# Kernel optimization log

Measured on AMD Instinct MI355X. Metric: run time of the kernel, lower is better.

## Reference

```python
import jax, jax.numpy as jnp
import numpy as np

NEG = -1e30  # mask value safe for logsumexp/max
HALF_POS = 4   # positive window: [t-4, t+4)
HALF_ALL = 16  # combined window: [t-16, t+16) (pos + 12 negatives each side)


def _normalize(x, axis=-1, eps=1e-12):
    # matches torch F.normalize: x / max(||x||, eps)
    n = jnp.linalg.norm(x, axis=axis, keepdims=True)
    return x / jnp.maximum(n, eps)


def _banded_logits(q, k, temperature):
    # q, k: [B, T, D] (normalized). Returns logits [B, T, W], valid mask, pos mask.
    B, T, D = q.shape
    offsets = jnp.arange(-HALF_ALL, HALF_ALL)          # [W=32]
    j = jnp.arange(T)[:, None] + offsets[None, :]      # [T, W] absolute indices
    valid = (j >= 0) & (j < T)                         # combined (pos+neg) window
    jc = jnp.clip(j, 0, T - 1)
    kg = k[:, jc, :]                                   # [B, T, W, D]
    logits = jnp.einsum('btd,btwd->btw', q, kg) / temperature
    pos = valid & (offsets >= -HALF_POS)[None, :] & (offsets < HALF_POS)[None, :]
    return logits, valid, pos


def _direction(q, k, temperature):
    logits, valid, pos = _banded_logits(q, k, temperature)
    lse_all = jax.nn.logsumexp(jnp.where(valid, logits, NEG), axis=2)  # [B, T]
    lse_pos = jax.nn.logsumexp(jnp.where(pos, logits, NEG), axis=2)    # [B, T]
    # per-t loss is mean over batch; summed over t
    loss_sum = jnp.sum(jnp.mean(lse_all - lse_pos, axis=0))
    max_all = jnp.max(jnp.where(valid, logits, NEG), axis=2)
    max_pos = jnp.max(jnp.where(pos, logits, NEG), axis=2)
    # argmax falls in positive block (positives listed first -> ties go positive)
    correct = jnp.sum((max_pos >= max_all).astype(jnp.float32))
    return loss_sum, correct


def setup_inputs() -> dict:
    key = jax.random.key(0)
    k1, k2 = jax.random.split(key)
    B, T, D = 16, 4096, 128
    return {
        'motion_feature': jax.random.normal(k1, (B, T, D), dtype=jnp.float32),
        'audio_feature': jax.random.normal(k2, (B, T, D), dtype=jnp.float32),
    }


def reference(motion_feature, audio_feature):
    temperature = 0.1
    B, T, D = motion_feature.shape
    m = _normalize(motion_feature, axis=2)
    a = _normalize(audio_feature, axis=2)
    m2a_loss, m2a_correct = _direction(m, a, temperature)
    a2m_loss, a2m_correct = _direction(a, m, temperature)
    final_loss = (m2a_loss + a2m_loss) / (2 * T)
    total_correct = (m2a_correct + a2m_correct) / (2 * T * B)
    return final_loss, total_correct
```

## Files before the change

kernel.cpp:

```cpp
#include <hip/hip_runtime.h>
#include <hip/hip_bf16.h>

typedef __attribute__((ext_vector_type(8))) short bf16x8;
typedef __attribute__((ext_vector_type(4))) float f32x4;

#define T_DIM 4096
#define B_DIM 16
#define D_DIM 128
#define TILE 64
#define NTILE 4
#define ROWS 96
#define SROW 136
#define TBUF (ROWS * SROW)
#define NEGV -1e30f
#define NBLK 256
#define SCALE (1.0f / 131072.0f)

#define LDS_BARRIER() asm volatile("s_waitcnt lgkmcnt(0)\n\ts_barrier" ::: "memory")

__global__ __launch_bounds__(512, 2) void lcl_main(
    const float* __restrict__ mot, const float* __restrict__ aud,
    float* __restrict__ ws)
{
    __shared__ unsigned short sbuf[2 * 2 * TBUF];
    __shared__ float redL[8], redC[8];

    const int tid  = threadIdx.x;
    const int lane = tid & 63;
    const int wv   = tid >> 6;
    const int g32  = tid >> 5;
    const int l32  = tid & 31;

    const int lin = blockIdx.x;
    const int swz = (lin & 7) * (NBLK / 8) + (lin >> 3);
    const int by  = swz >> 4;
    const int tg  = swz & 15;
    const int tbase = tg * (NTILE * TILE);
    const size_t base = (size_t)by * (T_DIM * D_DIM);
    const bool edge = (tg == 0) || (tg == 15);

    const int dir = wv >> 2;
    const int mi  = wv & 3;

    const int fr    = lane & 15;
    const int fch   = (lane >> 4) * 8;
    const int col16 = lane & 15;
    const int g     = lane >> 4;

    float4 vm[6], va[6];
    auto issue = [&](int tstart) {
        const size_t off = base + (size_t)(tstart - 16 + g32) * D_DIM + l32 * 4;
        const float* spm = mot + off;
        const float* spa = aud + off;
        if (!edge) {
            #pragma unroll
            for (int i = 0; i < 6; ++i) {
                vm[i] = *reinterpret_cast<const float4*>(spm + (size_t)(16 * i) * D_DIM);
                va[i] = *reinterpret_cast<const float4*>(spa + (size_t)(16 * i) * D_DIM);
            }
        } else {
            #pragma unroll
            for (int i = 0; i < 6; ++i) {
                const bool ok = (unsigned)(tstart - 16 + g32 + 16 * i) < (unsigned)T_DIM;
                vm[i] = make_float4(0.f, 0.f, 0.f, 0.f);
                va[i] = vm[i];
                if (ok) {
                    vm[i] = *reinterpret_cast<const float4*>(spm + (size_t)(16 * i) * D_DIM);
                    va[i] = *reinterpret_cast<const float4*>(spa + (size_t)(16 * i) * D_DIM);
                }
            }
        }
    };

    issue(tbase);

    float lossW = 0.f, corrW = 0.f;

    #pragma unroll
    for (int tile = 0; tile < NTILE; ++tile) {
        const int t0  = tbase + tile * TILE;
        const int cur = tile & 1;
        unsigned short* smc = sbuf + (cur * 2 + 0) * TBUF;
        unsigned short* sac = sbuf + (cur * 2 + 1) * TBUF;

        {
            unsigned short* dpm = smc + g32 * SROW + l32 * 4;
            unsigned short* dpa = sac + g32 * SROW + l32 * 4;
            #pragma unroll
            for (int i = 0; i < 6; ++i) {
                union { __hip_bfloat16 h[4]; uint2 u; } pm, pa;
                pm.h[0] = __float2bfloat16(vm[i].x);
                pm.h[1] = __float2bfloat16(vm[i].y);
                pm.h[2] = __float2bfloat16(vm[i].z);
                pm.h[3] = __float2bfloat16(vm[i].w);
                pa.h[0] = __float2bfloat16(va[i].x);
                pa.h[1] = __float2bfloat16(va[i].y);
                pa.h[2] = __float2bfloat16(va[i].z);
                pa.h[3] = __float2bfloat16(va[i].w);
                *reinterpret_cast<uint2*>(dpm + 16 * i * SROW) = pm.u;
                *reinterpret_cast<uint2*>(dpa + 16 * i * SROW) = pa.u;
            }
        }

        if (tile + 1 < NTILE) issue(t0 + TILE);

        LDS_BARRIER();

        const unsigned short* q = (dir ? sac : smc);
        const unsigned short* k = (dir ? smc : sac);
        f32x4 acc0 = {0.f,0.f,0.f,0.f}, acc1 = acc0, acc2 = acc0;
        f32x4 n0 = acc0, n1 = acc0, n2 = acc0, nq = acc0;
        const unsigned short* qrow = q + (16 * (mi + 1) + fr) * SROW + fch;
        const unsigned short* k0   = k + ((mi + 0) * 16 + fr) * SROW + fch;
        const unsigned short* k1   = k + ((mi + 1) * 16 + fr) * SROW + fch;
        const unsigned short* k2   = k + ((mi + 2) * 16 + fr) * SROW + fch;
        #pragma unroll
        for (int ks = 0; ks < 4; ++ks) {
            bf16x8 bq = *reinterpret_cast<const bf16x8*>(qrow + ks * 32);
            bf16x8 a0 = *reinterpret_cast<const bf16x8*>(k0   + ks * 32);
            bf16x8 a1 = *reinterpret_cast<const bf16x8*>(k1   + ks * 32);
            bf16x8 a2 = *reinterpret_cast<const bf16x8*>(k2   + ks * 32);
            acc0 = __builtin_amdgcn_mfma_f32_16x16x32_bf16(a0, bq, acc0, 0, 0, 0);
            acc1 = __builtin_amdgcn_mfma_f32_16x16x32_bf16(a1, bq, acc1, 0, 0, 0);
            acc2 = __builtin_amdgcn_mfma_f32_16x16x32_bf16(a2, bq, acc2, 0, 0, 0);
            n0   = __builtin_amdgcn_mfma_f32_16x16x32_bf16(a0, a0, n0, 0, 0, 0);
            n1   = __builtin_amdgcn_mfma_f32_16x16x32_bf16(a1, a1, n1, 0, 0, 0);
            n2   = __builtin_amdgcn_mfma_f32_16x16x32_bf16(a2, a2, n2, 0, 0, 0);
            nq   = __builtin_amdgcn_mfma_f32_16x16x32_bf16(bq, bq, nq, 0, 0, 0);
        }

        const int rs = col16 & 3;
        const float dq = (rs == 0) ? nq[0] : (rs == 1) ? nq[1] : (rs == 2) ? nq[2] : nq[3];
        const float d0 = (rs == 0) ? n0[0] : (rs == 1) ? n0[1] : (rs == 2) ? n0[2] : n0[3];
        const float d1 = (rs == 0) ? n1[0] : (rs == 1) ? n1[1] : (rs == 2) ? n1[2] : n1[3];
        const float d2 = (rs == 0) ? n2[0] : (rs == 1) ? n2[1] : (rs == 2) ? n2[2] : n2[3];
        const float iq = rsqrtf(fmaxf(dq, 1e-24f));
        const float i0 = rsqrtf(fmaxf(d0, 1e-24f));
        const float i1 = rsqrtf(fmaxf(d1, 1e-24f));
        const float i2 = rsqrtf(fmaxf(d2, 1e-24f));

        const float scq10 = 10.0f * __shfl(iq, col16 + 16 * (col16 >> 2));
        const int srcn = 20 * g;
        f32x4 sck0, sck1, sck2;
        #pragma unroll
        for (int r = 0; r < 4; ++r) {
            sck0[r] = __shfl(i0, srcn + r);
            sck1[r] = __shfl(i1, srcn + r);
            sck2[r] = __shfl(i2, srcn + r);
        }

        const int jbase  = t0 - 16 + 16 * mi + 4 * g;
        const int kkbase = 4 * g - col16;

        float lv[12];
        bool  pmk[12];
        float mx = NEGV, mxp = NEGV;
        #pragma unroll
        for (int bb = 0; bb < 3; ++bb) {
            const f32x4 acc = (bb == 0) ? acc0 : ((bb == 1) ? acc1 : acc2);
            const f32x4 sck = (bb == 0) ? sck0 : ((bb == 1) ? sck1 : sck2);
            #pragma unroll
            for (int r = 0; r < 4; ++r) {
                const int kk = kkbase + 16 * bb + r;
                const int jg = jbase  + 16 * bb + r;
                const bool ok = ((unsigned)kk < 32u) && ((unsigned)jg < (unsigned)T_DIM);
                const float li = ok ? acc[r] * (scq10 * sck[r]) : NEGV;
                const bool  pi = ((unsigned)(kk - 12) < 8u);
                lv[bb * 4 + r]  = li;
                pmk[bb * 4 + r] = pi;
                mx  = fmaxf(mx, li);
                mxp = pi ? fmaxf(mxp, li) : mxp;
            }
        }
        mx  = fmaxf(mx,  __shfl_xor(mx,  16));
        mx  = fmaxf(mx,  __shfl_xor(mx,  32));
        mxp = fmaxf(mxp, __shfl_xor(mxp, 16));
        mxp = fmaxf(mxp, __shfl_xor(mxp, 32));

        float s = 0.f, sp = 0.f;
        #pragma unroll
        for (int i = 0; i < 12; ++i) {
            const float e = __expf(lv[i] - mx);
            s  += e;
            sp += pmk[i] ? e : 0.f;
        }
        s  += __shfl_xor(s,  16);  s  += __shfl_xor(s,  32);
        sp += __shfl_xor(sp, 16);  sp += __shfl_xor(sp, 32);

        if (g == 0) {
            lossW += __logf(s / sp);
            corrW += (mxp >= mx) ? 1.0f : 0.0f;
        }
    }

    #pragma unroll
    for (int m = 32; m; m >>= 1) {
        lossW += __shfl_xor(lossW, m);
        corrW += __shfl_xor(corrW, m);
    }
    if (lane == 0) { redL[wv] = lossW; redC[wv] = corrW; }
    __syncthreads();
    if (tid == 0) {
        float L = 0.f, C = 0.f;
        #pragma unroll
        for (int i = 0; i < 8; ++i) { L += redL[i]; C += redC[i]; }
        ws[2 * swz]     = L;
        ws[2 * swz + 1] = C;
    }
}

__global__ __launch_bounds__(256) void lcl_final(
    const float* __restrict__ ws, float* __restrict__ out)
{
    const int tid = threadIdx.x;
    const float2 v = reinterpret_cast<const float2*>(ws)[tid];
    float L = v.x, C = v.y;
    #pragma unroll
    for (int m = 32; m; m >>= 1) { L += __shfl_xor(L, m); C += __shfl_xor(C, m); }
    __shared__ float rl[4], rc[4];
    if ((tid & 63) == 0) { rl[tid >> 6] = L; rc[tid >> 6] = C; }
    __syncthreads();
    if (tid == 0) {
        out[0] = (rl[0] + rl[1] + rl[2] + rl[3]) * SCALE;
        out[1] = (rc[0] + rc[1] + rc[2] + rc[3]) * SCALE;
    }
}

extern "C" void kernel_launch(void* const* d_in, const int* in_sizes, int n_in,
                              void* d_out, int out_size, void* d_ws, size_t ws_size,
                              hipStream_t stream) {
    const float* mot = (const float*)d_in[0];
    const float* aud = (const float*)d_in[1];
    float* out = (float*)d_out;
    float* ws  = (float*)d_ws;

    lcl_main<<<NBLK, 512, 0, stream>>>(mot, aud, ws);
    lcl_final<<<1, 256, 0, stream>>>(ws, out);
}
```

Measured before the change: 21.44 us.

## Double block count with half tiles per block and single-buffered LDS

Splits the time axis into 32 groups per batch instead of 16, so 512 blocks each process 2 tiles rather than 256 blocks processing 4. The LDS double buffer is dropped for one buffer per input, with an extra barrier after the MFMA loads so the next tile's stores cannot overwrite data still being read. The final reduction becomes a single wave summing 512 partials. This is meant to fill more CUs and cut LDS use, which may allow more resident blocks. In exchange, each block recomputes a larger share of halo rows and pays an extra barrier per tile.

Result: slower. 22.80 us (+6.4%).

```diff
diff --git a/kernel.cpp b/kernel.cpp
--- a/kernel.cpp
+++ b/kernel.cpp
@@ -8,12 +8,11 @@
 #define B_DIM 16
 #define D_DIM 128
 #define TILE 64
-#define NTILE 4
+#define NTILE 2
 #define ROWS 96
 #define SROW 136
-#define TBUF (ROWS * SROW)
 #define NEGV -1e30f
-#define NBLK 256
+#define NBLK 512
 #define SCALE (1.0f / 131072.0f)
 
 #define LDS_BARRIER() asm volatile("s_waitcnt lgkmcnt(0)\n\ts_barrier" ::: "memory")
@@ -22,7 +21,8 @@
     const float* __restrict__ mot, const float* __restrict__ aud,
     float* __restrict__ ws)
 {
-    __shared__ unsigned short sbuf[2 * 2 * TBUF];
+    __shared__ unsigned short sm[ROWS * SROW];
+    __shared__ unsigned short sa[ROWS * SROW];
     __shared__ float redL[8], redC[8];
 
     const int tid  = threadIdx.x;
@@ -33,11 +33,11 @@
 
     const int lin = blockIdx.x;
     const int swz = (lin & 7) * (NBLK / 8) + (lin >> 3);
-    const int by  = swz >> 4;
-    const int tg  = swz & 15;
+    const int by  = swz >> 5;
+    const int tg  = swz & 31;
     const int tbase = tg * (NTILE * TILE);
     const size_t base = (size_t)by * (T_DIM * D_DIM);
-    const bool edge = (tg == 0) || (tg == 15);
+    const bool edge = (tg == 0) || (tg == 31);
 
     const int dir = wv >> 2;
     const int mi  = wv & 3;
@@ -78,14 +78,11 @@
 
     #pragma unroll
     for (int tile = 0; tile < NTILE; ++tile) {
-        const int t0  = tbase + tile * TILE;
-        const int cur = tile & 1;
-        unsigned short* smc = sbuf + (cur * 2 + 0) * TBUF;
-        unsigned short* sac = sbuf + (cur * 2 + 1) * TBUF;
+        const int t0 = tbase + tile * TILE;
 
         {
-            unsigned short* dpm = smc + g32 * SROW + l32 * 4;
-            unsigned short* dpa = sac + g32 * SROW + l32 * 4;
+            unsigned short* dpm = sm + g32 * SROW + l32 * 4;
+            unsigned short* dpa = sa + g32 * SROW + l32 * 4;
             #pragma unroll
             for (int i = 0; i < 6; ++i) {
                 union { __hip_bfloat16 h[4]; uint2 u; } pm, pa;
@@ -106,8 +103,8 @@
 
         LDS_BARRIER();
 
-        const unsigned short* q = (dir ? sac : smc);
-        const unsigned short* k = (dir ? smc : sac);
+        const unsigned short* q = (dir ? sa : sm);
+        const unsigned short* k = (dir ? sm : sa);
         f32x4 acc0 = {0.f,0.f,0.f,0.f}, acc1 = acc0, acc2 = acc0;
         f32x4 n0 = acc0, n1 = acc0, n2 = acc0, nq = acc0;
         const unsigned short* qrow = q + (16 * (mi + 1) + fr) * SROW + fch;
@@ -129,6 +126,8 @@
             nq   = __builtin_amdgcn_mfma_f32_16x16x32_bf16(bq, bq, nq, 0, 0, 0);
         }
 
+        if (tile + 1 < NTILE) LDS_BARRIER();
+
         const int rs = col16 & 3;
         const float dq = (rs == 0) ? nq[0] : (rs == 1) ? nq[1] : (rs == 2) ? nq[2] : nq[3];
         const float d0 = (rs == 0) ? n0[0] : (rs == 1) ? n0[1] : (rs == 2) ? n0[2] : n0[3];
@@ -209,20 +208,23 @@
     }
 }
 
-__global__ __launch_bounds__(256) void lcl_final(
+__global__ __launch_bounds__(64) void lcl_final(
     const float* __restrict__ ws, float* __restrict__ out)
 {
     const int tid = threadIdx.x;
-    const float2 v = reinterpret_cast<const float2*>(ws)[tid];
-    float L = v.x, C = v.y;
+    const float2* w2 = reinterpret_cast<const float2*>(ws);
+    float L = 0.f, C = 0.f;
+    #pragma unroll
+    for (int i = 0; i < 8; ++i) {
+        const float2 v = w2[tid + i * 64];
+        L += v.x;
+        C += v.y;
+    }
     #pragma unroll
     for (int m = 32; m; m >>= 1) { L += __shfl_xor(L, m); C += __shfl_xor(C, m); }
-    __shared__ float rl[4], rc[4];
-    if ((tid & 63) == 0) { rl[tid >> 6] = L; rc[tid >> 6] = C; }
-    __syncthreads();
     if (tid == 0) {
-        out[0] = (rl[0] + rl[1] + rl[2] + rl[3]) * SCALE;
-        out[1] = (rc[0] + rc[1] + rc[2] + rc[3]) * SCALE;
+        out[0] = L * SCALE;
+        out[1] = C * SCALE;
     }
 }
 
@@ -235,5 +237,5 @@
     float* ws  = (float*)d_ws;
 
     lcl_main<<<NBLK, 512, 0, stream>>>(mot, aud, ws);
-    lcl_final<<<1, 256, 0, stream>>>(ws, out);
+    lcl_final<<<1, 64, 0, stream>>>(ws, out);
 }
```
